# Kernel optimization log

Hardware: AMD Instinct MI355X
Metric: run time of the kernel (lower is better)

Reference implementation:

```python
import jax, jax.numpy as jnp
import numpy as np
from jax import lax

B, H, W, C, NH = 16, 64, 64, 192, 6


def rope2d(x, h, w, c, base=10000.0):
    # 2D RoPE: channel_dims=(h,w), k_max = c // 4; angles (h,w,c//2)
    kmax = c // 4
    theta = 1.0 / (base ** (jnp.arange(kmax, dtype=jnp.float32) / kmax))
    ai = jnp.broadcast_to(jnp.arange(h, dtype=jnp.float32)[:, None, None] * theta, (h, w, kmax))
    aj = jnp.broadcast_to(jnp.arange(w, dtype=jnp.float32)[None, :, None] * theta, (h, w, kmax))
    ang = jnp.concatenate([ai, aj], axis=-1)  # (h,w,c//2)
    cos, sin = jnp.cos(ang), jnp.sin(ang)
    xr = x.reshape(*x.shape[:-1], c // 2, 2)
    xe, xo = xr[..., 0], xr[..., 1]
    # complex multiply (cos + i sin) * (xe + i xo)
    return jnp.stack([xe * cos - xo * sin, xe * sin + xo * cos], axis=-1).reshape(x.shape)


def setup_inputs() -> dict:
    key = jax.random.key(0)
    ks = jax.random.split(key, 4)
    return {
        "x": jax.random.normal(ks[0], (B, H, W, C), dtype=jnp.float32),
        "qk_w": jax.random.normal(ks[1], (2 * C, C), dtype=jnp.float32) * 0.02,
        "qk_b": jnp.zeros((2 * C,), dtype=jnp.float32),
        "lepe_w": jax.random.normal(ks[2], (C, 1, 3, 3), dtype=jnp.float32) * 0.1,
        "lepe_b": jnp.zeros((C,), dtype=jnp.float32),
    }


def reference(x, qk_w, qk_b, lepe_w, lepe_b):
    b, h, w, c = x.shape
    n = h * w
    nh = NH
    d = c // nh
    qk = x @ qk_w.T + qk_b  # (b,h,w,2c)
    q = jax.nn.elu(qk[..., :c]) + 1.0
    k = jax.nn.elu(qk[..., c:]) + 1.0
    q_rope = rope2d(q, h, w, c).reshape(b, n, nh, d).transpose(0, 2, 1, 3)  # (b,nh,n,d)
    k_rope = rope2d(k, h, w, c).reshape(b, n, nh, d).transpose(0, 2, 1, 3)
    qh = q.reshape(b, n, nh, d).transpose(0, 2, 1, 3)
    kh = k.reshape(b, n, nh, d).transpose(0, 2, 1, 3)
    vh = x.reshape(b, n, nh, d).transpose(0, 2, 1, 3)  # v = x
    kmean = kh.mean(axis=2)  # (b,nh,d)
    z = 1.0 / (jnp.einsum('bhnd,bhd->bhn', qh, kmean)[..., None] + 1e-6)  # (b,nh,n,1)
    scale = 1.0 / jnp.sqrt(jnp.float32(n))
    kv = jnp.einsum('bhnd,bhne->bhde', k_rope * scale, vh * scale)  # (b,nh,d,d)
    out = jnp.einsum('bhnd,bhde->bhne', q_rope, kv) * z  # (b,nh,n,d)
    out = out.transpose(0, 2, 1, 3).reshape(b, n, c)
    # LePE: depthwise 3x3 conv on v (= x) in NCHW
    v_nchw = x.transpose(0, 3, 1, 2)
    lepe = lax.conv_general_dilated(v_nchw, lepe_w, (1, 1), 'SAME',
                                    dimension_numbers=('NCHW', 'OIHW', 'NCHW'),
                                    feature_group_count=c)
    lepe = lepe + lepe_b[None, :, None, None]
    return out + lepe.transpose(0, 2, 3, 1).reshape(b, n, c)
```

## Files before the change

kernel.cpp:

```cpp
#include <hip/hip_runtime.h>
#include <hip/hip_bf16.h>

using short8   = __attribute__((ext_vector_type(8))) short;
using floatx4  = __attribute__((ext_vector_type(4))) float;
using floatx16 = __attribute__((ext_vector_type(16))) float;

#define CC 192
#define CN 4096
#define NHEAD 6
#define DHEAD 32
#define NZERO (16 * NHEAD * DHEAD * DHEAD + 16 * NHEAD * DHEAD)
#define ZBLK ((NZERO + 255) / 256)
#define TABN 12

__device__ __forceinline__ float bf2f(short s) {
    return __uint_as_float(((unsigned)(unsigned short)s) << 16);
}
__device__ __forceinline__ short f2bf(float f) {
    __hip_bfloat16 h = __float2bfloat16(f);
    return *(short*)&h;
}

__global__ void k0_all(float* __restrict__ zp, unsigned* __restrict__ tabs,
                       const float* __restrict__ qkw, __hip_bfloat16* __restrict__ wfr)
{
    int bid = blockIdx.x;
    if (bid < ZBLK) {
        int i = bid * 256 + threadIdx.x;
        if (i < NZERO) zp[i] = 0.f;
    } else if (bid < ZBLK + TABN) {
        int idx = (bid - ZBLK) * 256 + threadIdx.x;
        if (idx >= 64 * 48) return;
        int pos = idx / 48, i = idx - pos * 48;
        float theta = expf(-(float)i * (9.210340371976184f / 48.0f));
        float ang = (float)pos * theta;
        unsigned c = (unsigned)(unsigned short)f2bf(cosf(ang));
        unsigned s = (unsigned)(unsigned short)f2bf(sinf(ang));
        tabs[idx] = c | (s << 16);
    } else {
        int tid = (bid - ZBLK - TABN) * 256 + threadIdx.x;
        if (tid >= 24 * 6 * 64) return;
        int lane = tid & 63;
        int ks = (tid >> 6) % 6;
        int nig = tid / (6 * 64);
        int col = nig * 16 + (lane & 15);
        int k = ks * 32 + (lane >> 4) * 8;
        const float4* src = (const float4*)(qkw + (long)col * CC + k);
        float4 f0 = src[0], f1 = src[1];
        short8 s;
        s[0] = f2bf(f0.x); s[1] = f2bf(f0.y); s[2] = f2bf(f0.z); s[3] = f2bf(f0.w);
        s[4] = f2bf(f1.x); s[5] = f2bf(f1.y); s[6] = f2bf(f1.z); s[7] = f2bf(f1.w);
        *(short8*)&wfr[(long)tid * 8] = s;
    }
}

__global__ __launch_bounds__(512)
void k1_gemm(const float* __restrict__ x, const __hip_bfloat16* __restrict__ wfr,
             const float* __restrict__ qkb,
             __hip_bfloat16* __restrict__ qws, __hip_bfloat16* __restrict__ kws,
             __hip_bfloat16* __restrict__ xbf)
{
    __shared__ __align__(16) short A_lds[128 * 200];
    __shared__ __align__(16) short B_lds[24 * 512];

    const int tid  = threadIdx.x;
    const int wid  = tid >> 6, lane = tid & 63;
    const int wm   = wid >> 1, wn = wid & 1;
    const int lrow = lane & 15;
    const int l4   = lane >> 4;
    const long rowBase = (long)blockIdx.x * 128;

#pragma unroll
    for (int it = 0; it < 6; ++it) {
        int slot = it * 512 + tid;
        int row = slot / 24, c0 = (slot - (slot / 24) * 24) * 8;
        const float4* src = (const float4*)(x + (rowBase + row) * CC + c0);
        float4 f0 = src[0], f1 = src[1];
        short8 s;
        s[0] = f2bf(f0.x); s[1] = f2bf(f0.y); s[2] = f2bf(f0.z); s[3] = f2bf(f0.w);
        s[4] = f2bf(f1.x); s[5] = f2bf(f1.y); s[6] = f2bf(f1.z); s[7] = f2bf(f1.w);
        *(short8*)&A_lds[row * 200 + c0] = s;
        *(short8*)&xbf[(rowBase + row) * CC + c0] = s;
    }

    floatx4 acc[2][12];
#pragma unroll
    for (int i = 0; i < 2; ++i)
#pragma unroll
        for (int j = 0; j < 12; ++j) acc[i][j] = (floatx4)0.f;

    for (int ks = 0; ks < 6; ++ks) {
        short8 bst[3];
#pragma unroll
        for (int j = 0; j < 3; ++j) {
            int s = j * 512 + tid;
            bst[j] = *(const short8*)&wfr[((long)((s >> 6) * 6 + ks) * 64 + (s & 63)) * 8];
        }
        __syncthreads();
#pragma unroll
        for (int j = 0; j < 3; ++j) {
            int s = j * 512 + tid;
            *(short8*)&B_lds[s * 8] = bst[j];
        }
        __syncthreads();

        short8 a0 = *(const short8*)&A_lds[(wm * 32 + lrow) * 200 + ks * 32 + l4 * 8];
        short8 a1 = *(const short8*)&A_lds[(wm * 32 + 16 + lrow) * 200 + ks * 32 + l4 * 8];
#pragma unroll
        for (int ni = 0; ni < 12; ++ni) {
            short8 bf = *(const short8*)&B_lds[(wn * 12 + ni) * 512 + lane * 8];
            acc[0][ni] = __builtin_amdgcn_mfma_f32_16x16x32_bf16(a0, bf, acc[0][ni], 0, 0, 0);
            acc[1][ni] = __builtin_amdgcn_mfma_f32_16x16x32_bf16(a1, bf, acc[1][ni], 0, 0, 0);
        }
    }

    __hip_bfloat16* dstbase = wn ? kws : qws;
#pragma unroll
    for (int ni = 0; ni < 12; ++ni) {
        int col_l = ni * 16 + lrow;
        float bias = qkb[wn * 192 + col_l];
#pragma unroll
        for (int mi = 0; mi < 2; ++mi) {
#pragma unroll
            for (int r = 0; r < 4; ++r) {
                int rowl = wm * 32 + mi * 16 + l4 * 4 + r;
                long rowg = rowBase + rowl;
                float v = acc[mi][ni][r] + bias;
                v = (v > 0.f) ? (v + 1.f) : __expf(v);
                dstbase[rowg * CC + col_l] = __float2bfloat16(v);
            }
        }
    }
}

__global__ __launch_bounds__(256)
void k2_kv(const __hip_bfloat16* __restrict__ kws, const __hip_bfloat16* __restrict__ xbf,
           const unsigned* __restrict__ tabs, float* __restrict__ kv, float* __restrict__ kmean)
{
    int bid = blockIdx.x;
    int chunk = bid & 7;
    int hd = (bid >> 3) % NHEAD;
    int b = bid / (8 * NHEAD);
    int tid = threadIdx.x;
    int lane = tid & 63, wave = tid >> 6;

    __shared__ __align__(16) short S[8192];
    __shared__ float km_s[32];
    char* krT = (char*)S;
    char* vT  = (char*)S + 8192;

    if (tid < 32) km_s[tid] = 0.f;

    const int krow = tid >> 2, kq = tid & 3;

    floatx16 acc = (floatx16)0.f;
    float msum[8];
#pragma unroll
    for (int j = 0; j < 8; ++j) msum[j] = 0.f;

    const int n0 = chunk * 512;
    const long rb = (long)b * CN;

    short8 k8[2], v8[2];
#pragma unroll
    for (int p = 0; p < 2; ++p) {
        int n = n0 + p * 64 + krow;
        k8[p] = *(const short8*)&kws[(rb + n) * CC + hd * DHEAD + kq * 8];
        v8[p] = *(const short8*)&xbf[(rb + n) * CC + hd * DHEAD + kq * 8];
    }

    for (int batch = 0; batch < 4; ++batch) {
        if (batch) __syncthreads();
#pragma unroll
        for (int p = 0; p < 2; ++p) {
            int r = p * 64 + krow;
            int nbase = n0 + batch * 128 + p * 64;
            int hpos = nbase >> 6;
            uint4 u = (hd < 3)
                ? *(const uint4*)&tabs[hpos * 48 + hd * 16 + kq * 4]
                : *(const uint4*)&tabs[krow * 48 + (hd - 3) * 16 + kq * 4];
            float kf[8];
#pragma unroll
            for (int j = 0; j < 8; ++j) { kf[j] = bf2f(k8[p][j]); msum[j] += kf[j]; }
            float cs[4], sn[4];
            cs[0] = bf2f((short)(u.x & 0xffff)); sn[0] = bf2f((short)(u.x >> 16));
            cs[1] = bf2f((short)(u.y & 0xffff)); sn[1] = bf2f((short)(u.y >> 16));
            cs[2] = bf2f((short)(u.z & 0xffff)); sn[2] = bf2f((short)(u.z >> 16));
            cs[3] = bf2f((short)(u.w & 0xffff)); sn[3] = bf2f((short)(u.w >> 16));
            short kr8[8];
#pragma unroll
            for (int q = 0; q < 4; ++q) {
                kr8[2*q]   = f2bf(kf[2*q] * cs[q] - kf[2*q+1] * sn[q]);
                kr8[2*q+1] = f2bf(kf[2*q] * sn[q] + kf[2*q+1] * cs[q]);
            }
#pragma unroll
            for (int j = 0; j < 8; ++j) {
                int ch = kq * 8 + j;
                int g = j ^ (kq << 1);
                int byte = (ch * 256 + r * 2) ^ (g << 4);
                *(short*)(krT + byte) = kr8[j];
                *(short*)(vT  + byte) = v8[p][j];
            }
        }
        if (batch < 3) {
#pragma unroll
            for (int p = 0; p < 2; ++p) {
                int n = n0 + (batch + 1) * 128 + p * 64 + krow;
                k8[p] = *(const short8*)&kws[(rb + n) * CC + hd * DHEAD + kq * 8];
                v8[p] = *(const short8*)&xbf[(rb + n) * CC + hd * DHEAD + kq * 8];
            }
        }
        __syncthreads();
        const int d = lane & 31;
        const int kh = (lane >> 5) * 8;
        const int gd = (d & 7) ^ (((d >> 3) & 3) << 1);
#pragma unroll
        for (int s = 0; s < 2; ++s) {
            int k = wave * 32 + s * 16 + kh;
            int abyte = (d * 256 + k * 2) ^ (gd << 4);
            short8 af = *(const short8*)(krT + abyte);
            short8 bf = *(const short8*)(vT + abyte);
            acc = __builtin_amdgcn_mfma_f32_32x32x16_bf16(af, bf, acc, 0, 0, 0);
        }
    }
    __syncthreads();

    float* red = (float*)S;
#pragma unroll
    for (int r = 0; r < 16; ++r)
        red[(wave * 16 + r) * 64 + lane] = acc[r];
#pragma unroll
    for (int j = 0; j < 8; ++j) {
        float m = msum[j];
        m += __shfl_down(m, 32);
        m += __shfl_down(m, 16);
        m += __shfl_down(m, 8);
        m += __shfl_down(m, 4);
        if (lane < 4) atomicAdd(&km_s[(tid & 3) * 8 + j], m);
    }
    __syncthreads();

    const float sc = 1.f / 4096.f;
    {
        float* kvb = kv + (long)(b * NHEAD + hd) * DHEAD * DHEAD;
        const int l = tid & 63;
        const int rbase = (tid >> 6) * 4;
#pragma unroll
        for (int i = 0; i < 4; ++i) {
            int r = rbase + i;
            float v = red[(0 * 16 + r) * 64 + l] + red[(1 * 16 + r) * 64 + l]
                    + red[(2 * 16 + r) * 64 + l] + red[(3 * 16 + r) * 64 + l];
            int row = (r & 3) + 8 * (r >> 2) + 4 * (l >> 5);
            int col = l & 31;
            atomicAdd(&kvb[row * DHEAD + col], v * sc);
        }
    }
    if (tid < 32) atomicAdd(&kmean[(b * NHEAD + hd) * DHEAD + tid], km_s[tid] * sc);
}

__global__ __launch_bounds__(256)
void k3_out(const __hip_bfloat16* __restrict__ qws, const __hip_bfloat16* __restrict__ xbf,
            const unsigned* __restrict__ tabs, const float* __restrict__ kv,
            const float* __restrict__ kmean, const float* __restrict__ lw,
            const float* __restrict__ lb, float* __restrict__ out)
{
    int raw = blockIdx.x;
    int bid = (raw & 7) * 128 + (raw >> 3);
    int b = bid >> 6, h = bid & 63;
    int tid = threadIdx.x;
    int wave = tid >> 6, lane = tid & 63, lrow = lane & 15, l4 = lane >> 4;

    __shared__ __align__(16) __hip_bfloat16 qa[64][104];
    __shared__ __align__(16) __hip_bfloat16 kvt[NHEAD][32][36];
    __shared__ __align__(16) float lwT[9][192];
    __shared__ float lb_lds[CC];
    __shared__ float km_lds[CC];
    __shared__ float zden[64][8];

    const long nbase = (long)b * CN + h * 64;

    const float* kvsrc = kv + (long)b * NHEAD * DHEAD * DHEAD;
    for (int i = tid; i < NHEAD * DHEAD * DHEAD; i += 256) {
        int hd = i >> 10, d = (i >> 5) & 31, e = i & 31;
        kvt[hd][e][d] = __float2bfloat16(kvsrc[i]);
    }
    if (tid < CC) { km_lds[tid] = kmean[b * CC + tid]; lb_lds[tid] = lb[tid]; }
    for (int i = tid; i < CC * 9; i += 256) {
        int c = i / 9, tap = i - c * 9;
        lwT[tap][c] = lw[i];
    }
    __syncthreads();

#pragma unroll
    for (int half = 0; half < 2; ++half) {
#pragma unroll
        for (int it = 0; it < 3; ++it) {
            int slot = it * 256 + tid;
            int w = slot / 12;
            int sub = slot - w * 12;
            int c0 = half * 96 + sub * 8;
            short8 qv = *(const short8*)&qws[(nbase + w) * CC + c0];
            float q[8];
#pragma unroll
            for (int j = 0; j < 8; ++j) q[j] = bf2f(qv[j]);
            float p = 0.f;
#pragma unroll
            for (int j = 0; j < 8; ++j) p += q[j] * km_lds[c0 + j];
            p += __shfl_xor(p, 1);
            p += __shfl_xor(p, 2);
            if ((sub & 3) == 0) zden[w][half * 3 + (sub >> 2)] = p;
            uint4 u = (half == 0)
                ? *(const uint4*)&tabs[h * 48 + sub * 4]
                : *(const uint4*)&tabs[w * 48 + sub * 4];
            float4 t0, t1;
            t0.x = bf2f((short)(u.x & 0xffff)); t0.y = bf2f((short)(u.x >> 16));
            t0.z = bf2f((short)(u.y & 0xffff)); t0.w = bf2f((short)(u.y >> 16));
            t1.x = bf2f((short)(u.z & 0xffff)); t1.y = bf2f((short)(u.z >> 16));
            t1.z = bf2f((short)(u.w & 0xffff)); t1.w = bf2f((short)(u.w >> 16));
            short8 qr;
            qr[0] = f2bf(q[0]*t0.x - q[1]*t0.y);  qr[1] = f2bf(q[0]*t0.y + q[1]*t0.x);
            qr[2] = f2bf(q[2]*t0.z - q[3]*t0.w);  qr[3] = f2bf(q[2]*t0.w + q[3]*t0.z);
            qr[4] = f2bf(q[4]*t1.x - q[5]*t1.y);  qr[5] = f2bf(q[4]*t1.y + q[5]*t1.x);
            qr[6] = f2bf(q[6]*t1.z - q[7]*t1.w);  qr[7] = f2bf(q[6]*t1.w + q[7]*t1.z);
            *(short8*)&qa[w][sub * 8] = qr;
        }
        __syncthreads();

        const int rt = wave;
        const int wbase = rt * 16 + l4 * 4;
#pragma unroll
        for (int hl = 0; hl < 3; ++hl) {
            int hd = half * 3 + hl;
            short8 a = *(const short8*)&qa[rt * 16 + lrow][hl * 32 + l4 * 8];
            float zv[4];
#pragma unroll
            for (int r = 0; r < 4; ++r) zv[r] = 1.f / (zden[wbase + r][hd] + 1e-6f);
#pragma unroll
            for (int nt = 0; nt < 2; ++nt) {
                short8 bfr = *(const short8*)&kvt[hd][nt * 16 + lrow][l4 * 8];
                floatx4 acc = __builtin_amdgcn_mfma_f32_16x16x32_bf16(a, bfr, (floatx4)0.f, 0, 0, 0);
                int col_l = hl * 32 + nt * 16 + lrow;
#pragma unroll
                for (int r = 0; r < 4; ++r)
                    qa[wbase + r][col_l] = __float2bfloat16(acc[r] * zv[r]);
            }
        }
        __syncthreads();

#pragma unroll
        for (int it = 0; it < 3; ++it) {
            int slot = it * 256 + tid;
            int w = slot / 12;
            int g = slot - w * 12;
            int c0g = g * 8;
            int c0 = half * 96 + c0g;
            float vals[8];
#pragma unroll
            for (int j = 0; j < 8; ++j) vals[j] = lb_lds[c0 + j];
#pragma unroll
            for (int dy = 0; dy < 3; ++dy) {
                int hy = h + dy - 1;
                if (hy < 0 || hy > 63) continue;
                const short* base = (const short*)xbf + (((long)b * 64 + hy) * 64) * CC + c0;
#pragma unroll
                for (int dx = 0; dx < 3; ++dx) {
                    int wx = w + dx - 1;
                    if (wx < 0 || wx > 63) continue;
                    short8 xv = *(const short8*)&base[(long)wx * CC];
                    const float4* wt4 = (const float4*)&lwT[dy * 3 + dx][c0];
                    float4 wa = wt4[0], wb = wt4[1];
                    vals[0] += bf2f(xv[0]) * wa.x;  vals[1] += bf2f(xv[1]) * wa.y;
                    vals[2] += bf2f(xv[2]) * wa.z;  vals[3] += bf2f(xv[3]) * wa.w;
                    vals[4] += bf2f(xv[4]) * wb.x;  vals[5] += bf2f(xv[5]) * wb.y;
                    vals[6] += bf2f(xv[6]) * wb.z;  vals[7] += bf2f(xv[7]) * wb.w;
                }
            }
            short8 at = *(const short8*)&qa[w][c0g];
#pragma unroll
            for (int j = 0; j < 8; ++j) vals[j] += bf2f(at[j]);
            float4 o0, o1;
            o0.x = vals[0]; o0.y = vals[1]; o0.z = vals[2]; o0.w = vals[3];
            o1.x = vals[4]; o1.y = vals[5]; o1.z = vals[6]; o1.w = vals[7];
            float* op = &out[(nbase + w) * CC + c0];
            *(float4*)op = o0;
            *(float4*)(op + 4) = o1;
        }
        __syncthreads();
    }
}

extern "C" void kernel_launch(void* const* d_in, const int* in_sizes, int n_in,
                              void* d_out, int out_size, void* d_ws, size_t ws_size,
                              hipStream_t stream)
{
    const float* x   = (const float*)d_in[0];
    const float* qkw = (const float*)d_in[1];
    const float* qkb = (const float*)d_in[2];
    const float* lw  = (const float*)d_in[3];
    const float* lb  = (const float*)d_in[4];
    float* out = (float*)d_out;

    char* ws = (char*)d_ws;
    unsigned* tabs = (unsigned*)ws;            ws += (size_t)64 * 48 * 4;
    __hip_bfloat16* qws = (__hip_bfloat16*)ws; ws += (size_t)16 * CN * CC * 2;
    __hip_bfloat16* kws = (__hip_bfloat16*)ws; ws += (size_t)16 * CN * CC * 2;
    __hip_bfloat16* xbf = (__hip_bfloat16*)ws; ws += (size_t)16 * CN * CC * 2;
    __hip_bfloat16* wfr = (__hip_bfloat16*)ws; ws += (size_t)24 * 6 * 64 * 8 * 2;
    float* kv = (float*)ws;                    ws += (size_t)16 * NHEAD * DHEAD * DHEAD * 4;
    float* km = (float*)ws;                    ws += (size_t)16 * NHEAD * DHEAD * 4;

    const int wblk = (24 * 6 * 64 + 255) / 256;
    k0_all<<<ZBLK + TABN + wblk, 256, 0, stream>>>(kv, tabs, qkw, wfr);
    k1_gemm<<<512, 512, 0, stream>>>(x, wfr, qkb, qws, kws, xbf);
    k2_kv<<<16 * NHEAD * 8, 256, 0, stream>>>(kws, xbf, tabs, kv, km);
    k3_out<<<16 * 64, 256, 0, stream>>>(qws, xbf, tabs, kv, km, lw, lb, out);
}
```

Before: 85.06 us.

## Fuse K-V outer-product reduction into QK GEMM epilogue, drop k workspace

The separate k2_kv kernel is removed. The GEMM kernel now applies ELU+1 and RoPE to its k tile in registers, writes it transposed into LDS, and computes the per-head K^T·V partials with MFMA on that tile. Partials go to global memory via atomics, along with the k-mean sums. This avoids writing and rereading the bf16 k buffer and saves one launch. In exchange the GEMM tail gains a serialized six-head loop with many barriers and only two waves doing MFMA. Each block now issues more atomics (128-row chunks instead of 512). A transposed rotation table is added so the w-position lookups can be vector loads.

```diff
diff --git a/kernel.cpp b/kernel.cpp
--- a/kernel.cpp
+++ b/kernel.cpp
@@ -22,6 +22,7 @@
 }
 
 __global__ void k0_all(float* __restrict__ zp, unsigned* __restrict__ tabs,
+                       unsigned* __restrict__ tabsT,
                        const float* __restrict__ qkw, __hip_bfloat16* __restrict__ wfr)
 {
     int bid = blockIdx.x;
@@ -32,11 +33,13 @@
         int idx = (bid - ZBLK) * 256 + threadIdx.x;
         if (idx >= 64 * 48) return;
         int pos = idx / 48, i = idx - pos * 48;
-        float theta = expf(-(float)i * (9.210340371976184f / 48.0f));
+        float theta = __expf(-(float)i * (9.210340371976184f / 48.0f));
         float ang = (float)pos * theta;
         unsigned c = (unsigned)(unsigned short)f2bf(cosf(ang));
         unsigned s = (unsigned)(unsigned short)f2bf(sinf(ang));
-        tabs[idx] = c | (s << 16);
+        unsigned packed = c | (s << 16);
+        tabs[idx] = packed;
+        tabsT[i * 64 + pos] = packed;
     } else {
         int tid = (bid - ZBLK - TABN) * 256 + threadIdx.x;
         if (tid >= 24 * 6 * 64) return;
@@ -56,9 +59,10 @@
 
 __global__ __launch_bounds__(512)
 void k1_gemm(const float* __restrict__ x, const __hip_bfloat16* __restrict__ wfr,
-             const float* __restrict__ qkb,
-             __hip_bfloat16* __restrict__ qws, __hip_bfloat16* __restrict__ kws,
-             __hip_bfloat16* __restrict__ xbf)
+             const float* __restrict__ qkb, const unsigned* __restrict__ tabs,
+             const unsigned* __restrict__ tabsT,
+             __hip_bfloat16* __restrict__ qws, __hip_bfloat16* __restrict__ xbf,
+             float* __restrict__ kv, float* __restrict__ km)
 {
     __shared__ __align__(16) short A_lds[128 * 200];
     __shared__ __align__(16) short B_lds[24 * 512];
@@ -69,6 +73,8 @@
     const int lrow = lane & 15;
     const int l4   = lane >> 4;
     const long rowBase = (long)blockIdx.x * 128;
+    const int b   = blockIdx.x >> 5;
+    const int H0  = (blockIdx.x & 31) * 2;
 
 #pragma unroll
     for (int it = 0; it < 6; ++it) {
@@ -114,148 +120,130 @@
         }
     }
 
-    __hip_bfloat16* dstbase = wn ? kws : qws;
-#pragma unroll
-    for (int ni = 0; ni < 12; ++ni) {
-        int col_l = ni * 16 + lrow;
-        float bias = qkb[wn * 192 + col_l];
-#pragma unroll
-        for (int mi = 0; mi < 2; ++mi) {
-#pragma unroll
-            for (int r = 0; r < 4; ++r) {
-                int rowl = wm * 32 + mi * 16 + l4 * 4 + r;
-                long rowg = rowBase + rowl;
-                float v = acc[mi][ni][r] + bias;
-                v = (v > 0.f) ? (v + 1.f) : __expf(v);
-                dstbase[rowg * CC + col_l] = __float2bfloat16(v);
-            }
-        }
-    }
-}
-
-__global__ __launch_bounds__(256)
-void k2_kv(const __hip_bfloat16* __restrict__ kws, const __hip_bfloat16* __restrict__ xbf,
-           const unsigned* __restrict__ tabs, float* __restrict__ kv, float* __restrict__ kmean)
-{
-    int bid = blockIdx.x;
-    int chunk = bid & 7;
-    int hd = (bid >> 3) % NHEAD;
-    int b = bid / (8 * NHEAD);
-    int tid = threadIdx.x;
-    int lane = tid & 63, wave = tid >> 6;
-
-    __shared__ __align__(16) short S[8192];
-    __shared__ float km_s[32];
-    char* krT = (char*)S;
-    char* vT  = (char*)S + 8192;
-
-    if (tid < 32) km_s[tid] = 0.f;
-
-    const int krow = tid >> 2, kq = tid & 3;
-
-    floatx16 acc = (floatx16)0.f;
-    float msum[8];
-#pragma unroll
-    for (int j = 0; j < 8; ++j) msum[j] = 0.f;
-
-    const int n0 = chunk * 512;
-    const long rb = (long)b * CN;
-
-    short8 k8[2], v8[2];
-#pragma unroll
-    for (int p = 0; p < 2; ++p) {
-        int n = n0 + p * 64 + krow;
-        k8[p] = *(const short8*)&kws[(rb + n) * CC + hd * DHEAD + kq * 8];
-        v8[p] = *(const short8*)&xbf[(rb + n) * CC + hd * DHEAD + kq * 8];
-    }
-
-    for (int batch = 0; batch < 4; ++batch) {
-        if (batch) __syncthreads();
-#pragma unroll
-        for (int p = 0; p < 2; ++p) {
-            int r = p * 64 + krow;
-            int nbase = n0 + batch * 128 + p * 64;
-            int hpos = nbase >> 6;
-            uint4 u = (hd < 3)
-                ? *(const uint4*)&tabs[hpos * 48 + hd * 16 + kq * 4]
-                : *(const uint4*)&tabs[krow * 48 + (hd - 3) * 16 + kq * 4];
-            float kf[8];
-#pragma unroll
-            for (int j = 0; j < 8; ++j) { kf[j] = bf2f(k8[p][j]); msum[j] += kf[j]; }
-            float cs[4], sn[4];
-            cs[0] = bf2f((short)(u.x & 0xffff)); sn[0] = bf2f((short)(u.x >> 16));
-            cs[1] = bf2f((short)(u.y & 0xffff)); sn[1] = bf2f((short)(u.y >> 16));
-            cs[2] = bf2f((short)(u.z & 0xffff)); sn[2] = bf2f((short)(u.z >> 16));
-            cs[3] = bf2f((short)(u.w & 0xffff)); sn[3] = bf2f((short)(u.w >> 16));
-            short kr8[8];
-#pragma unroll
-            for (int q = 0; q < 4; ++q) {
-                kr8[2*q]   = f2bf(kf[2*q] * cs[q] - kf[2*q+1] * sn[q]);
-                kr8[2*q+1] = f2bf(kf[2*q] * sn[q] + kf[2*q+1] * cs[q]);
-            }
+    if (wn == 0) {
+#pragma unroll
+        for (int ni = 0; ni < 12; ++ni) {
+            int col = ni * 16 + lrow;
+            float bias = qkb[col];
+#pragma unroll
+            for (int mi = 0; mi < 2; ++mi)
+#pragma unroll
+                for (int r = 0; r < 4; ++r) {
+                    int rowl = wm * 32 + mi * 16 + l4 * 4 + r;
+                    float v = acc[mi][ni][r] + bias;
+                    v = (v > 0.f) ? (v + 1.f) : __expf(v);
+                    qws[(rowBase + rowl) * CC + col] = __float2bfloat16(v);
+                }
+        }
+    }
+    __syncthreads();
+
+    char* krT = (char*)B_lds;
+    char* vT  = (char*)B_lds + 8192;
+    float* red = (float*)((char*)B_lds + 16384);
+    float* kvb = kv + (long)b * NHEAD * DHEAD * DHEAD;
+    const float sc = 1.f / 4096.f;
+    const int odd = lrow & 1;
+
+#pragma unroll
+    for (int hd = 0; hd < 6; ++hd) {
+        if (hd > 0) {
+#pragma unroll
+            for (int i2 = 0; i2 < 2; ++i2) {
+                int idx = i2 * 512 + tid;
+                int r = idx >> 6, l = idx & 63;
+                float v = red[r * 64 + l] + red[(16 + r) * 64 + l];
+                int row = (r & 3) + 8 * (r >> 2) + 4 * (l >> 5);
+                atomicAdd(&kvb[(hd - 1) * 1024 + row * DHEAD + (l & 31)], v * sc);
+            }
+        }
+        if (wn == 1) {
+#pragma unroll
+            for (int nisub = 0; nisub < 2; ++nisub) {
+                const int ni = hd * 2 + nisub;
+                int col = ni * 16 + lrow;
+                float bias = qkb[192 + col];
+                int ch = nisub * 16 + lrow;
+                int g = (ch & 7) ^ ((ch >> 3) << 1);
+                float csv[2][4], snv[2][4];
+                if (hd < 3) {
+                    unsigned u = tabs[(H0 + (wm >> 1)) * 48 + (col >> 1)];
+                    float cs = bf2f((short)(u & 0xffff)), sn = bf2f((short)(u >> 16));
+#pragma unroll
+                    for (int mi = 0; mi < 2; ++mi)
+#pragma unroll
+                        for (int r = 0; r < 4; ++r) { csv[mi][r] = cs; snv[mi][r] = sn; }
+                } else {
+                    int i = (col >> 1) - 48;
+#pragma unroll
+                    for (int mi = 0; mi < 2; ++mi) {
+                        int pos0 = (wm & 1) * 32 + mi * 16 + l4 * 4;
+                        uint4 u = *(const uint4*)&tabsT[i * 64 + pos0];
+                        csv[mi][0] = bf2f((short)(u.x & 0xffff)); snv[mi][0] = bf2f((short)(u.x >> 16));
+                        csv[mi][1] = bf2f((short)(u.y & 0xffff)); snv[mi][1] = bf2f((short)(u.y >> 16));
+                        csv[mi][2] = bf2f((short)(u.z & 0xffff)); snv[mi][2] = bf2f((short)(u.z >> 16));
+                        csv[mi][3] = bf2f((short)(u.w & 0xffff)); snv[mi][3] = bf2f((short)(u.w >> 16));
+                    }
+                }
+                float kms = 0.f;
+#pragma unroll
+                for (int mi = 0; mi < 2; ++mi)
+#pragma unroll
+                    for (int r = 0; r < 4; ++r) {
+                        int n = wm * 32 + mi * 16 + l4 * 4 + r;
+                        float v = acc[mi][ni][r] + bias;
+                        v = (v > 0.f) ? (v + 1.f) : __expf(v);
+                        kms += v;
+                        float p = __shfl_xor(v, 1);
+                        float o = odd ? (p * snv[mi][r] + v * csv[mi][r])
+                                      : (v * csv[mi][r] - p * snv[mi][r]);
+                        int byte = (ch * 256 + n * 2) ^ (g << 4);
+                        *(short*)(krT + byte) = f2bf(o);
+                    }
+                kms += __shfl_xor(kms, 16);
+                kms += __shfl_xor(kms, 32);
+                if (lane < 16) atomicAdd(&km[b * CC + col], kms * sc);
+            }
+        }
+        {
+            int n = tid >> 2, chg = tid & 3;
+            short8 v8 = *(const short8*)&A_lds[n * 200 + hd * 32 + chg * 8];
 #pragma unroll
             for (int j = 0; j < 8; ++j) {
-                int ch = kq * 8 + j;
-                int g = j ^ (kq << 1);
-                int byte = (ch * 256 + r * 2) ^ (g << 4);
-                *(short*)(krT + byte) = kr8[j];
-                *(short*)(vT  + byte) = v8[p][j];
-            }
-        }
-        if (batch < 3) {
-#pragma unroll
-            for (int p = 0; p < 2; ++p) {
-                int n = n0 + (batch + 1) * 128 + p * 64 + krow;
-                k8[p] = *(const short8*)&kws[(rb + n) * CC + hd * DHEAD + kq * 8];
-                v8[p] = *(const short8*)&xbf[(rb + n) * CC + hd * DHEAD + kq * 8];
-            }
-        }
-        __syncthreads();
-        const int d = lane & 31;
-        const int kh = (lane >> 5) * 8;
-        const int gd = (d & 7) ^ (((d >> 3) & 3) << 1);
-#pragma unroll
-        for (int s = 0; s < 2; ++s) {
-            int k = wave * 32 + s * 16 + kh;
-            int abyte = (d * 256 + k * 2) ^ (gd << 4);
-            short8 af = *(const short8*)(krT + abyte);
-            short8 bf = *(const short8*)(vT + abyte);
-            acc = __builtin_amdgcn_mfma_f32_32x32x16_bf16(af, bf, acc, 0, 0, 0);
-        }
-    }
-    __syncthreads();
-
-    float* red = (float*)S;
-#pragma unroll
-    for (int r = 0; r < 16; ++r)
-        red[(wave * 16 + r) * 64 + lane] = acc[r];
-#pragma unroll
-    for (int j = 0; j < 8; ++j) {
-        float m = msum[j];
-        m += __shfl_down(m, 32);
-        m += __shfl_down(m, 16);
-        m += __shfl_down(m, 8);
-        m += __shfl_down(m, 4);
-        if (lane < 4) atomicAdd(&km_s[(tid & 3) * 8 + j], m);
-    }
-    __syncthreads();
-
-    const float sc = 1.f / 4096.f;
-    {
-        float* kvb = kv + (long)(b * NHEAD + hd) * DHEAD * DHEAD;
-        const int l = tid & 63;
-        const int rbase = (tid >> 6) * 4;
-#pragma unroll
-        for (int i = 0; i < 4; ++i) {
-            int r = rbase + i;
-            float v = red[(0 * 16 + r) * 64 + l] + red[(1 * 16 + r) * 64 + l]
-                    + red[(2 * 16 + r) * 64 + l] + red[(3 * 16 + r) * 64 + l];
-            int row = (r & 3) + 8 * (r >> 2) + 4 * (l >> 5);
-            int col = l & 31;
-            atomicAdd(&kvb[row * DHEAD + col], v * sc);
-        }
-    }
-    if (tid < 32) atomicAdd(&kmean[(b * NHEAD + hd) * DHEAD + tid], km_s[tid] * sc);
+                int ch = chg * 8 + j;
+                int g2 = j ^ (chg << 1);
+                int byte = (ch * 256 + n * 2) ^ (g2 << 4);
+                *(short*)(vT + byte) = v8[j];
+            }
+        }
+        __syncthreads();
+        if (wid < 2) {
+            floatx16 kacc = (floatx16)0.f;
+            const int d = lane & 31;
+            const int kh = (lane >> 5) * 8;
+            const int gd = (d & 7) ^ (((d >> 3) & 3) << 1);
+#pragma unroll
+            for (int s = 0; s < 4; ++s) {
+                int k = wid * 64 + s * 16 + kh;
+                int abyte = (d * 256 + k * 2) ^ (gd << 4);
+                short8 af = *(const short8*)(krT + abyte);
+                short8 bf = *(const short8*)(vT + abyte);
+                kacc = __builtin_amdgcn_mfma_f32_32x32x16_bf16(af, bf, kacc, 0, 0, 0);
+            }
+#pragma unroll
+            for (int r = 0; r < 16; ++r)
+                red[(wid * 16 + r) * 64 + lane] = kacc[r];
+        }
+        __syncthreads();
+    }
+#pragma unroll
+    for (int i2 = 0; i2 < 2; ++i2) {
+        int idx = i2 * 512 + tid;
+        int r = idx >> 6, l = idx & 63;
+        float v = red[r * 64 + l] + red[(16 + r) * 64 + l];
+        int row = (r & 3) + 8 * (r >> 2) + 4 * (l >> 5);
+        atomicAdd(&kvb[5 * 1024 + row * DHEAD + (l & 31)], v * sc);
+    }
 }
 
 __global__ __launch_bounds__(256)
@@ -401,17 +389,16 @@
     float* out = (float*)d_out;
 
     char* ws = (char*)d_ws;
-    unsigned* tabs = (unsigned*)ws;            ws += (size_t)64 * 48 * 4;
+    unsigned* tabs  = (unsigned*)ws;           ws += (size_t)64 * 48 * 4;
+    unsigned* tabsT = (unsigned*)ws;           ws += (size_t)48 * 64 * 4;
     __hip_bfloat16* qws = (__hip_bfloat16*)ws; ws += (size_t)16 * CN * CC * 2;
-    __hip_bfloat16* kws = (__hip_bfloat16*)ws; ws += (size_t)16 * CN * CC * 2;
     __hip_bfloat16* xbf = (__hip_bfloat16*)ws; ws += (size_t)16 * CN * CC * 2;
     __hip_bfloat16* wfr = (__hip_bfloat16*)ws; ws += (size_t)24 * 6 * 64 * 8 * 2;
     float* kv = (float*)ws;                    ws += (size_t)16 * NHEAD * DHEAD * DHEAD * 4;
     float* km = (float*)ws;                    ws += (size_t)16 * NHEAD * DHEAD * 4;
 
     const int wblk = (24 * 6 * 64 + 255) / 256;
-    k0_all<<<ZBLK + TABN + wblk, 256, 0, stream>>>(kv, tabs, qkw, wfr);
-    k1_gemm<<<512, 512, 0, stream>>>(x, wfr, qkb, qws, kws, xbf);
-    k2_kv<<<16 * NHEAD * 8, 256, 0, stream>>>(kws, xbf, tabs, kv, km);
+    k0_all<<<ZBLK + TABN + wblk, 256, 0, stream>>>(kv, tabs, tabsT, qkw, wfr);
+    k1_gemm<<<512, 512, 0, stream>>>(x, wfr, qkb, tabs, tabsT, qws, xbf, kv, km);
     k3_out<<<16 * 64, 256, 0, stream>>>(qws, xbf, tabs, kv, km, lw, lb, out);
 }
```

After: 99.58 us. 1.17x slower.
